# Optimization experiments

Measured on AMD Instinct MI355X. Metric: run time of the kernel, lower is better.

## Reference

```python
import jax, jax.numpy as jnp
import numpy as np

EPS = 1e-12

def _normalize(v):
    n = jnp.linalg.norm(v, axis=-1, keepdims=True)
    return v / jnp.maximum(n, EPS)

def _bgs(J):
    # J: [b, N, D, 3, 2] -> rotation matrices R [b, N, D, 3, 3]
    b1 = _normalize(J[..., :, 0])
    a2 = J[..., :, 1]
    dot = jnp.sum(b1 * a2, axis=-1, keepdims=True)
    b2 = _normalize(a2 - dot * b1)
    b3 = jnp.cross(b1, b2)
    return jnp.stack([b1, b2, b3], axis=-1)  # columns b1,b2,b3

def setup_inputs() -> dict:
    key = jax.random.key(0)
    k1, k2, k3, k4, k5 = jax.random.split(key, 5)
    B, N, D, OUT = 16, 4096, 64, 64
    X = jax.random.normal(k1, (B, N, D, 3), dtype=jnp.float32)
    J = jax.random.normal(k2, (B, N, D, 3, 2), dtype=jnp.float32)
    A = jax.random.normal(k3, (OUT, D), dtype=jnp.float32)
    Bm = jax.random.normal(k4, (OUT, D), dtype=jnp.float32)
    C = jax.random.normal(k5, (OUT, D), dtype=jnp.float32)
    return {"X": X, "J": J, "A": A, "Bm": Bm, "C": C}

def reference(X, J, A, Bm, C):
    R = _bgs(J)  # [b, N, D, 3, 3]
    # RT_i . X == column i of R dotted with X -> scalar per channel
    RTX = jnp.einsum('bndij,bndi->bndj', R, X)  # [b, N, D, 3], j-th entry = RT_j X
    rt0 = RTX[..., 0:1]
    rt1 = RTX[..., 1:2]
    rt2 = RTX[..., 2:3]
    col0 = R[..., :, 0]
    col1 = R[..., :, 1]
    col2 = R[..., :, 2]
    # a_term (after adding b_term, as in original forward)
    a_term = col1 * rt1 + col2 * rt2 + col2 * rt1 - col1 * rt2  # [b, N, D, 3]
    c_term = col0 * rt0
    Y = jnp.einsum('fe,bnei->bnfi', A, a_term) + jnp.einsum('fe,bnei->bnfi', C, c_term)
    Y = jnp.einsum('fe,bnei->bnfi', Bm, Y)
    return Y
```

## Files before the change

### kernel.cpp

```cpp
#include <hip/hip_runtime.h>


typedef __bf16 bf16x8 __attribute__((ext_vector_type(8)));
typedef float floatx4 __attribute__((ext_vector_type(4)));

#define RSW 68

__global__ __launch_bounds__(256) void prep_kernel(const float* __restrict__ A,
                                                   const float* __restrict__ Bm,
                                                   const float* __restrict__ C,
                                                   __bf16* __restrict__ acat) {
    int tid = blockIdx.x * 256 + threadIdx.x;
    int f = tid >> 6;
    int e = tid & 63;
    float m = 0.f, m2 = 0.f;
    #pragma unroll 8
    for (int k = 0; k < 64; ++k) {
        float b = Bm[f * 64 + k];
        m  = fmaf(b, A[k * 64 + e], m);
        m2 = fmaf(b, C[k * 64 + e], m2);
    }
    acat[f * 128 + 2 * e]     = (__bf16)m;
    acat[f * 128 + 2 * e + 1] = (__bf16)m2;
}

static __device__ __forceinline__ unsigned pk(float a, float c) {
    unsigned short ua = __builtin_bit_cast(unsigned short, (__bf16)a);
    unsigned short uc = __builtin_bit_cast(unsigned short, (__bf16)c);
    return ((unsigned)uc << 16) | ua;
}

__global__ __launch_bounds__(256, 4) void main_kernel(const float* __restrict__ X,
                                                      const float* __restrict__ J,
                                                      const __bf16* __restrict__ acat,
                                                      float* __restrict__ out) {
    __shared__ __align__(16) float buf[4][2304];

    const int wave = threadIdx.x >> 6;
    const int lane = threadIdx.x & 63;
    const int l15  = lane & 15;
    const int quad = lane >> 4;
    const int pb0  = blockIdx.x * 64 + wave * 4;

    float* stg = buf[wave];

    floatx4 jt[6], xt[3];
    {
        const floatx4* jg = (const floatx4*)(J + (size_t)pb0 * 384);
        const floatx4* xg = (const floatx4*)(X + (size_t)pb0 * 192);
        #pragma unroll
        for (int u = 0; u < 6; ++u) jt[u] = jg[u * 64 + lane];
        #pragma unroll
        for (int u = 0; u < 3; ++u) xt[u] = xg[u * 64 + lane];
    }

    #pragma unroll
    for (int t = 0; t < 4; ++t) {
        const int pbase = pb0 + t * 16;

        {
            floatx4* sj = (floatx4*)stg;
            floatx4* sx = (floatx4*)(stg + 1536);
            #pragma unroll
            for (int u = 0; u < 6; ++u) sj[u * 64 + lane] = jt[u];
            #pragma unroll
            for (int u = 0; u < 3; ++u) sx[u * 64 + lane] = xt[u];
        }

        if (t < 3) {
            const floatx4* jg = (const floatx4*)(J + (size_t)(pbase + 16) * 384);
            const floatx4* xg = (const floatx4*)(X + (size_t)(pbase + 16) * 192);
            #pragma unroll
            for (int u = 0; u < 6; ++u) jt[u] = jg[u * 64 + lane];
            #pragma unroll
            for (int u = 0; u < 3; ++u) xt[u] = xg[u * 64 + lane];
        }

        __asm__ volatile("s_waitcnt lgkmcnt(0)" ::: "memory");

        float2 ja, jb, jc; float xx, xy, xz;
        {
            const float* jst = stg + lane * 6;
            ja = *(const float2*)(jst);
            jb = *(const float2*)(jst + 2);
            jc = *(const float2*)(jst + 4);
            const float* xst = stg + 1536 + lane * 3;
            xx = xst[0]; xy = xst[1]; xz = xst[2];
        }
        #pragma unroll
        for (int pi = 0; pi < 4; ++pi) {
            float2 na = ja, nb = jb, nc = jc; float nx = xx, ny = xy, nz = xz;
            if (pi < 3) {
                const float* jst = stg + (pi + 1) * 384 + lane * 6;
                na = *(const float2*)(jst);
                nb = *(const float2*)(jst + 2);
                nc = *(const float2*)(jst + 4);
                const float* xst = stg + 1536 + (pi + 1) * 192 + lane * 3;
                nx = xst[0]; ny = xst[1]; nz = xst[2];
            }

            float a0x = ja.x, a0y = jb.x, a0z = jc.x;
            float a1x = ja.y, a1y = jb.y, a1z = jc.y;

            float n0 = sqrtf(a0x * a0x + a0y * a0y + a0z * a0z);
            float r0 = 1.0f / fmaxf(n0, 1e-12f);
            float b1x = a0x * r0, b1y = a0y * r0, b1z = a0z * r0;

            float d  = b1x * a1x + b1y * a1y + b1z * a1z;
            float ux = a1x - d * b1x, uy = a1y - d * b1y, uz = a1z - d * b1z;
            float n2 = sqrtf(ux * ux + uy * uy + uz * uz);
            float r2 = 1.0f / fmaxf(n2, 1e-12f);
            float b2x = ux * r2, b2y = uy * r2, b2z = uz * r2;

            float b3x = b1y * b2z - b1z * b2y;
            float b3y = b1z * b2x - b1x * b2z;
            float b3z = b1x * b2y - b1y * b2x;

            float rt0 = b1x * xx + b1y * xy + b1z * xz;
            float rt1 = b2x * xx + b2y * xy + b2z * xz;
            float rt2 = b3x * xx + b3y * xy + b3z * xz;

            float s = rt1 - rt2, tt = rt1 + rt2;

            unsigned* zr = (unsigned*)(stg + pi * 396);
            zr[lane]           = pk(b2x * s + b3x * tt, b1x * rt0);
            zr[RSW + lane]     = pk(b2y * s + b3y * tt, b1y * rt0);
            zr[2 * RSW + lane] = pk(b2z * s + b3z * tt, b1z * rt0);

            ja = na; jb = nb; jc = nc; xx = nx; xy = ny; xz = nz;
        }

        __asm__ volatile("s_waitcnt lgkmcnt(0)" ::: "memory");

        const __bf16* ap = acat;
        __asm__ volatile("" : "+s"(ap));
        bf16x8 afrag[4][4];
        #pragma unroll
        for (int mt = 0; mt < 4; ++mt)
            #pragma unroll
            for (int kc = 0; kc < 4; ++kc)
                afrag[mt][kc] = *(const bf16x8*)(ap + (mt * 16 + l15) * 128 + kc * 32 + quad * 8);

        floatx4 acc[4];
        #pragma unroll
        for (int mt = 0; mt < 4; ++mt) acc[mt] = (floatx4){0.f, 0.f, 0.f, 0.f};

        int row = l15 > 11 ? 11 : l15;
        int pz  = (row * 21846) >> 16;
        int iz  = row - pz * 3;
        const __bf16* zb = (const __bf16*)stg + pz * 792 + iz * 136;
        #pragma unroll
        for (int kc = 0; kc < 4; ++kc) {
            bf16x8 b = *(const bf16x8*)(zb + kc * 32 + quad * 8);
            #pragma unroll
            for (int mt = 0; mt < 4; ++mt)
                acc[mt] = __builtin_amdgcn_mfma_f32_16x16x32_bf16(afrag[mt][kc], b, acc[mt], 0, 0, 0);
        }

        __asm__ volatile("s_waitcnt lgkmcnt(0)" ::: "memory");

        float* dl = stg;
        #pragma unroll
        for (int mt = 0; mt < 4; ++mt) {
            int n = l15;
            if (n < 12) {
                int pl = (n * 21846) >> 16;
                int i  = n - pl * 3;
                float* dst = dl + pl * 196 + i;
                #pragma unroll
                for (int r = 0; r < 4; ++r) {
                    int f = mt * 16 + quad * 4 + r;
                    dst[f * 3] = acc[mt][r];
                }
            }
        }

        __asm__ volatile("s_waitcnt lgkmcnt(0)" ::: "memory");

        floatx4* og = (floatx4*)(out + (size_t)pbase * 192);
        #pragma unroll
        for (int u = 0; u < 3; ++u) {
            int g  = u * 64 + lane;
            int pg = (g * 1366) >> 16;
            int o  = g - pg * 48;
            og[g] = *(const floatx4*)(dl + pg * 196 + o * 4);
        }
    }
}

extern "C" void kernel_launch(void* const* d_in, const int* in_sizes, int n_in,
                              void* d_out, int out_size, void* d_ws, size_t ws_size,
                              hipStream_t stream) {
    const float* X  = (const float*)d_in[0];
    const float* J  = (const float*)d_in[1];
    const float* A  = (const float*)d_in[2];
    const float* Bm = (const float*)d_in[3];
    const float* C  = (const float*)d_in[4];
    float* out = (float*)d_out;
    __bf16* acat = (__bf16*)d_ws;

    prep_kernel<<<16, 256, 0, stream>>>(A, Bm, C, acat);

    main_kernel<<<1024, 256, 0, stream>>>(X, J, acat, out);
}
```

Baseline: 218.8 us.

## Drop per-wave multi-tile loop and launch four times more blocks

The main kernel no longer loops over four 16-position tiles per wave with register prefetch of the next tile. Each wave now handles one tile, and the grid grows from 1024 to 4096 blocks, so latency is hidden by more resident waves instead of software pipelining. The A-fragment loads are now repeated per block rather than amortized over four tiles. The prep kernel is relaunched with 64-thread blocks, which does not change the work it does.

```diff
diff --git a/kernel.cpp b/kernel.cpp
--- a/kernel.cpp
+++ b/kernel.cpp
@@ -6,11 +6,11 @@
 
 #define RSW 68
 
-__global__ __launch_bounds__(256) void prep_kernel(const float* __restrict__ A,
-                                                   const float* __restrict__ Bm,
-                                                   const float* __restrict__ C,
-                                                   __bf16* __restrict__ acat) {
-    int tid = blockIdx.x * 256 + threadIdx.x;
+__global__ __launch_bounds__(64) void prep_kernel(const float* __restrict__ A,
+                                                  const float* __restrict__ Bm,
+                                                  const float* __restrict__ C,
+                                                  __bf16* __restrict__ acat) {
+    int tid = blockIdx.x * 64 + threadIdx.x;
     int f = tid >> 6;
     int e = tid & 63;
     float m = 0.f, m2 = 0.f;
@@ -40,151 +40,132 @@
     const int lane = threadIdx.x & 63;
     const int l15  = lane & 15;
     const int quad = lane >> 4;
-    const int pb0  = blockIdx.x * 64 + wave * 4;
+    const int pbase = blockIdx.x * 16 + wave * 4;
 
     float* stg = buf[wave];
 
-    floatx4 jt[6], xt[3];
     {
-        const floatx4* jg = (const floatx4*)(J + (size_t)pb0 * 384);
-        const floatx4* xg = (const floatx4*)(X + (size_t)pb0 * 192);
+        const floatx4* jg = (const floatx4*)(J + (size_t)pbase * 384);
+        const floatx4* xg = (const floatx4*)(X + (size_t)pbase * 192);
+        floatx4 jt[6], xt[3];
         #pragma unroll
-        for (int u = 0; u < 6; ++u) jt[u] = jg[u * 64 + lane];
+        for (int t = 0; t < 6; ++t) jt[t] = jg[t * 64 + lane];
         #pragma unroll
-        for (int u = 0; u < 3; ++u) xt[u] = xg[u * 64 + lane];
+        for (int t = 0; t < 3; ++t) xt[t] = xg[t * 64 + lane];
+        floatx4* sj = (floatx4*)stg;
+        floatx4* sx = (floatx4*)(stg + 1536);
+        #pragma unroll
+        for (int t = 0; t < 6; ++t) sj[t * 64 + lane] = jt[t];
+        #pragma unroll
+        for (int t = 0; t < 3; ++t) sx[t * 64 + lane] = xt[t];
     }
 
+    __asm__ volatile("s_waitcnt lgkmcnt(0)" ::: "memory");
+
+    float2 ja, jb, jc; float xx, xy, xz;
+    {
+        const float* jst = stg + lane * 6;
+        ja = *(const float2*)(jst);
+        jb = *(const float2*)(jst + 2);
+        jc = *(const float2*)(jst + 4);
+        const float* xst = stg + 1536 + lane * 3;
+        xx = xst[0]; xy = xst[1]; xz = xst[2];
+    }
     #pragma unroll
-    for (int t = 0; t < 4; ++t) {
-        const int pbase = pb0 + t * 16;
-
-        {
-            floatx4* sj = (floatx4*)stg;
-            floatx4* sx = (floatx4*)(stg + 1536);
-            #pragma unroll
-            for (int u = 0; u < 6; ++u) sj[u * 64 + lane] = jt[u];
-            #pragma unroll
-            for (int u = 0; u < 3; ++u) sx[u * 64 + lane] = xt[u];
+    for (int pi = 0; pi < 4; ++pi) {
+        float2 na = ja, nb = jb, nc = jc; float nx = xx, ny = xy, nz = xz;
+        if (pi < 3) {
+            const float* jst = stg + (pi + 1) * 384 + lane * 6;
+            na = *(const float2*)(jst);
+            nb = *(const float2*)(jst + 2);
+            nc = *(const float2*)(jst + 4);
+            const float* xst = stg + 1536 + (pi + 1) * 192 + lane * 3;
+            nx = xst[0]; ny = xst[1]; nz = xst[2];
         }
 
-        if (t < 3) {
-            const floatx4* jg = (const floatx4*)(J + (size_t)(pbase + 16) * 384);
-            const floatx4* xg = (const floatx4*)(X + (size_t)(pbase + 16) * 192);
-            #pragma unroll
-            for (int u = 0; u < 6; ++u) jt[u] = jg[u * 64 + lane];
-            #pragma unroll
-            for (int u = 0; u < 3; ++u) xt[u] = xg[u * 64 + lane];
-        }
+        float a0x = ja.x, a0y = jb.x, a0z = jc.x;
+        float a1x = ja.y, a1y = jb.y, a1z = jc.y;
 
-        __asm__ volatile("s_waitcnt lgkmcnt(0)" ::: "memory");
+        float n0 = sqrtf(a0x * a0x + a0y * a0y + a0z * a0z);
+        float r0 = 1.0f / fmaxf(n0, 1e-12f);
+        float b1x = a0x * r0, b1y = a0y * r0, b1z = a0z * r0;
 
-        float2 ja, jb, jc; float xx, xy, xz;
-        {
-            const float* jst = stg + lane * 6;
-            ja = *(const float2*)(jst);
-            jb = *(const float2*)(jst + 2);
-            jc = *(const float2*)(jst + 4);
-            const float* xst = stg + 1536 + lane * 3;
-            xx = xst[0]; xy = xst[1]; xz = xst[2];
-        }
+        float d  = b1x * a1x + b1y * a1y + b1z * a1z;
+        float ux = a1x - d * b1x, uy = a1y - d * b1y, uz = a1z - d * b1z;
+        float n2 = sqrtf(ux * ux + uy * uy + uz * uz);
+        float r2 = 1.0f / fmaxf(n2, 1e-12f);
+        float b2x = ux * r2, b2y = uy * r2, b2z = uz * r2;
+
+        float b3x = b1y * b2z - b1z * b2y;
+        float b3y = b1z * b2x - b1x * b2z;
+        float b3z = b1x * b2y - b1y * b2x;
+
+        float rt0 = b1x * xx + b1y * xy + b1z * xz;
+        float rt1 = b2x * xx + b2y * xy + b2z * xz;
+        float rt2 = b3x * xx + b3y * xy + b3z * xz;
+
+        float s = rt1 - rt2, tt = rt1 + rt2;
+
+        unsigned* zr = (unsigned*)(stg + pi * 396);
+        zr[lane]           = pk(b2x * s + b3x * tt, b1x * rt0);
+        zr[RSW + lane]     = pk(b2y * s + b3y * tt, b1y * rt0);
+        zr[2 * RSW + lane] = pk(b2z * s + b3z * tt, b1z * rt0);
+
+        ja = na; jb = nb; jc = nc; xx = nx; xy = ny; xz = nz;
+    }
+
+    bf16x8 afrag[4][4];
+    #pragma unroll
+    for (int mt = 0; mt < 4; ++mt)
         #pragma unroll
-        for (int pi = 0; pi < 4; ++pi) {
-            float2 na = ja, nb = jb, nc = jc; float nx = xx, ny = xy, nz = xz;
-            if (pi < 3) {
-                const float* jst = stg + (pi + 1) * 384 + lane * 6;
-                na = *(const float2*)(jst);
-                nb = *(const float2*)(jst + 2);
-                nc = *(const float2*)(jst + 4);
-                const float* xst = stg + 1536 + (pi + 1) * 192 + lane * 3;
-                nx = xst[0]; ny = xst[1]; nz = xst[2];
-            }
+        for (int kc = 0; kc < 4; ++kc)
+            afrag[mt][kc] = *(const bf16x8*)(acat + (mt * 16 + l15) * 128 + kc * 32 + quad * 8);
 
-            float a0x = ja.x, a0y = jb.x, a0z = jc.x;
-            float a1x = ja.y, a1y = jb.y, a1z = jc.y;
+    __asm__ volatile("s_waitcnt lgkmcnt(0)" ::: "memory");
 
-            float n0 = sqrtf(a0x * a0x + a0y * a0y + a0z * a0z);
-            float r0 = 1.0f / fmaxf(n0, 1e-12f);
-            float b1x = a0x * r0, b1y = a0y * r0, b1z = a0z * r0;
+    floatx4 acc[4];
+    #pragma unroll
+    for (int mt = 0; mt < 4; ++mt) acc[mt] = (floatx4){0.f, 0.f, 0.f, 0.f};
 
-            float d  = b1x * a1x + b1y * a1y + b1z * a1z;
-            float ux = a1x - d * b1x, uy = a1y - d * b1y, uz = a1z - d * b1z;
-            float n2 = sqrtf(ux * ux + uy * uy + uz * uz);
-            float r2 = 1.0f / fmaxf(n2, 1e-12f);
-            float b2x = ux * r2, b2y = uy * r2, b2z = uz * r2;
-
-            float b3x = b1y * b2z - b1z * b2y;
-            float b3y = b1z * b2x - b1x * b2z;
-            float b3z = b1x * b2y - b1y * b2x;
-
-            float rt0 = b1x * xx + b1y * xy + b1z * xz;
-            float rt1 = b2x * xx + b2y * xy + b2z * xz;
-            float rt2 = b3x * xx + b3y * xy + b3z * xz;
-
-            float s = rt1 - rt2, tt = rt1 + rt2;
-
-            unsigned* zr = (unsigned*)(stg + pi * 396);
-            zr[lane]           = pk(b2x * s + b3x * tt, b1x * rt0);
-            zr[RSW + lane]     = pk(b2y * s + b3y * tt, b1y * rt0);
-            zr[2 * RSW + lane] = pk(b2z * s + b3z * tt, b1z * rt0);
-
-            ja = na; jb = nb; jc = nc; xx = nx; xy = ny; xz = nz;
-        }
-
-        __asm__ volatile("s_waitcnt lgkmcnt(0)" ::: "memory");
-
-        const __bf16* ap = acat;
-        __asm__ volatile("" : "+s"(ap));
-        bf16x8 afrag[4][4];
+    int row = l15 > 11 ? 11 : l15;
+    int pz  = (row * 21846) >> 16;
+    int iz  = row - pz * 3;
+    const __bf16* zb = (const __bf16*)stg + pz * 792 + iz * 136;
+    #pragma unroll
+    for (int kc = 0; kc < 4; ++kc) {
+        bf16x8 b = *(const bf16x8*)(zb + kc * 32 + quad * 8);
         #pragma unroll
         for (int mt = 0; mt < 4; ++mt)
+            acc[mt] = __builtin_amdgcn_mfma_f32_16x16x32_bf16(afrag[mt][kc], b, acc[mt], 0, 0, 0);
+    }
+
+    __asm__ volatile("s_waitcnt lgkmcnt(0)" ::: "memory");
+
+    float* dl = stg;
+    #pragma unroll
+    for (int mt = 0; mt < 4; ++mt) {
+        int n = l15;
+        if (n < 12) {
+            int pl = (n * 21846) >> 16;
+            int i  = n - pl * 3;
+            float* dst = dl + pl * 196 + i;
             #pragma unroll
-            for (int kc = 0; kc < 4; ++kc)
-                afrag[mt][kc] = *(const bf16x8*)(ap + (mt * 16 + l15) * 128 + kc * 32 + quad * 8);
-
-        floatx4 acc[4];
-        #pragma unroll
-        for (int mt = 0; mt < 4; ++mt) acc[mt] = (floatx4){0.f, 0.f, 0.f, 0.f};
-
-        int row = l15 > 11 ? 11 : l15;
-        int pz  = (row * 21846) >> 16;
-        int iz  = row - pz * 3;
-        const __bf16* zb = (const __bf16*)stg + pz * 792 + iz * 136;
-        #pragma unroll
-        for (int kc = 0; kc < 4; ++kc) {
-            bf16x8 b = *(const bf16x8*)(zb + kc * 32 + quad * 8);
-            #pragma unroll
-            for (int mt = 0; mt < 4; ++mt)
-                acc[mt] = __builtin_amdgcn_mfma_f32_16x16x32_bf16(afrag[mt][kc], b, acc[mt], 0, 0, 0);
-        }
-
-        __asm__ volatile("s_waitcnt lgkmcnt(0)" ::: "memory");
-
-        float* dl = stg;
-        #pragma unroll
-        for (int mt = 0; mt < 4; ++mt) {
-            int n = l15;
-            if (n < 12) {
-                int pl = (n * 21846) >> 16;
-                int i  = n - pl * 3;
-                float* dst = dl + pl * 196 + i;
-                #pragma unroll
-                for (int r = 0; r < 4; ++r) {
-                    int f = mt * 16 + quad * 4 + r;
-                    dst[f * 3] = acc[mt][r];
-                }
+            for (int r = 0; r < 4; ++r) {
+                int f = mt * 16 + quad * 4 + r;
+                dst[f * 3] = acc[mt][r];
             }
         }
+    }
 
-        __asm__ volatile("s_waitcnt lgkmcnt(0)" ::: "memory");
+    __asm__ volatile("s_waitcnt lgkmcnt(0)" ::: "memory");
 
-        floatx4* og = (floatx4*)(out + (size_t)pbase * 192);
-        #pragma unroll
-        for (int u = 0; u < 3; ++u) {
-            int g  = u * 64 + lane;
-            int pg = (g * 1366) >> 16;
-            int o  = g - pg * 48;
-            og[g] = *(const floatx4*)(dl + pg * 196 + o * 4);
-        }
+    floatx4* og = (floatx4*)(out + (size_t)pbase * 192);
+    #pragma unroll
+    for (int t = 0; t < 3; ++t) {
+        int g  = t * 64 + lane;
+        int pg = (g * 1366) >> 16;
+        int o  = g - pg * 48;
+        og[g] = *(const floatx4*)(dl + pg * 196 + o * 4);
     }
 }
 
@@ -199,7 +180,7 @@
     float* out = (float*)d_out;
     __bf16* acat = (__bf16*)d_ws;
 
-    prep_kernel<<<16, 256, 0, stream>>>(A, Bm, C, acat);
+    prep_kernel<<<64, 64, 0, stream>>>(A, Bm, C, acat);
 
-    main_kernel<<<1024, 256, 0, stream>>>(X, J, acat, out);
+    main_kernel<<<4096, 256, 0, stream>>>(X, J, acat, out);
 }
```

Measured after the change: 211.2 us. 3.5% less time.
